# Performance work log

Measured on AMD Instinct MI355X. Metric: run time of the kernel, lower is better.

## Reference

```python
import jax, jax.numpy as jnp
import numpy as np

# ---- config (matches init_kwargs) ----
B, N, D = 16, 300, 256
HEADS, HD = 8, D // 8
FF = 1024
HID = FF // 2                      # SwiGLU hidden
SPATIAL = [(80, 80), (40, 40), (20, 20), (10, 10)]
LVL = len(SPATIAL)
NP = 4                              # points per level
TP = LVL * NP                       # total sampling points = 16
L = sum(h * w for h, w in SPATIAL)  # 8400
EPS = 1e-6


def setup_inputs() -> dict:
    key = jax.random.key(0)
    ks = jax.random.split(key, 24)
    s = 0.02
    return {
        "target": jax.random.normal(ks[0], (B, N, D), jnp.float32),
        "reference_points": jax.random.uniform(ks[1], (B, N, 1, 4), jnp.float32, 0.05, 0.95),
        "memory": jax.random.normal(ks[2], (B, L, D), jnp.float32),
        # self-attention
        "qkv_w": jax.random.normal(ks[3], (3 * D, D), jnp.float32) * s,
        "qkv_b": jnp.zeros((3 * D,), jnp.float32),
        "out_w": jax.random.normal(ks[4], (D, D), jnp.float32) * s,
        "out_b": jnp.zeros((D,), jnp.float32),
        "norm1_w": jnp.ones((D,), jnp.float32),
        # deformable cross-attention
        "off_w": jax.random.normal(ks[5], (HEADS * TP * 2, D), jnp.float32) * s,
        "off_b": jax.random.normal(ks[6], (HEADS * TP * 2,), jnp.float32) * 0.1,
        "aw_w": jax.random.normal(ks[7], (HEADS * TP, D), jnp.float32) * s,
        "aw_b": jnp.zeros((HEADS * TP,), jnp.float32),
        "cout_w": jax.random.normal(ks[8], (D, D), jnp.float32) * s,
        "cout_b": jnp.zeros((D,), jnp.float32),
        "norm2_w": jnp.ones((D,), jnp.float32),
        # SwiGLU FFN
        "w13": jax.random.normal(ks[9], (2 * HID, D), jnp.float32) * s,
        "w13_b": jnp.zeros((2 * HID,), jnp.float32),
        "w2": jax.random.normal(ks[10], (D, HID), jnp.float32) * s,
        "w2_b": jnp.zeros((D,), jnp.float32),
        "norm3_w": jnp.ones((D,), jnp.float32),
    }


def rmsnorm(x, w):
    return x * jax.lax.rsqrt(jnp.mean(x * x, axis=-1, keepdims=True) + EPS) * w


def bilinear_sample(vflat, loc, H, W):
    """vflat: (BH, hd, H*W); loc: (BH, Q, 2) in [0,1]. grid_sample align_corners=False, zero pad."""
    x = loc[..., 0] * W - 0.5
    y = loc[..., 1] * H - 0.5
    x0 = jnp.floor(x); y0 = jnp.floor(y)
    dx = x - x0; dy = y - y0
    x0i = x0.astype(jnp.int32); y0i = y0.astype(jnp.int32)

    def gather(xi, yi, w):
        valid = (xi >= 0) & (xi < W) & (yi >= 0) & (yi < H)
        idx = jnp.clip(yi, 0, H - 1) * W + jnp.clip(xi, 0, W - 1)
        g = jnp.take_along_axis(vflat, idx[:, None, :], axis=2)  # (BH, hd, Q)
        return g * (w * valid)[:, None, :]

    return (gather(x0i, y0i, (1 - dx) * (1 - dy))
            + gather(x0i + 1, y0i, dx * (1 - dy))
            + gather(x0i, y0i + 1, (1 - dx) * dy)
            + gather(x0i + 1, y0i + 1, dx * dy))


def reference(target, reference_points, memory, qkv_w, qkv_b, out_w, out_b, norm1_w,
              off_w, off_b, aw_w, aw_b, cout_w, cout_b, norm2_w,
              w13, w13_b, w2, w2_b, norm3_w):
    # ---------- self-attention (query_pos_embed=None, attn_mask=None) ----------
    qkv = target @ qkv_w.T + qkv_b                    # (B,N,3D)
    qkv = qkv.reshape(B, N, 3, HEADS, HD).transpose(2, 0, 3, 1, 4)
    q, k, v = qkv[0], qkv[1], qkv[2]                  # (B,H,N,hd)
    attn = jax.nn.softmax(jnp.einsum("bhqd,bhkd->bhqk", q, k) / np.sqrt(HD), axis=-1)
    sa = jnp.einsum("bhqk,bhkd->bhqd", attn, v).transpose(0, 2, 1, 3).reshape(B, N, D)
    x = rmsnorm(target + (sa @ out_w.T + out_b), norm1_w)

    # ---------- deformable cross-attention ----------
    # value_op: memory -> per-head value (B,H,hd,L)
    val = memory.reshape(B, L, HEADS, HD).transpose(0, 2, 3, 1).reshape(B * HEADS, HD, L)

    offsets = (x @ off_w.T + off_b).reshape(B, N, HEADS, TP, 2)
    aw = jax.nn.softmax((x @ aw_w.T + aw_b).reshape(B, N, HEADS, TP), axis=-1)

    ref_xy = reference_points[:, :, :, None, :2]      # (B,N,1,1,2)
    ref_wh = reference_points[:, :, :, None, 2:]
    pts_scale = 1.0 / NP
    loc = ref_xy + offsets * pts_scale * ref_wh * 0.5  # (B,N,H,TP,2)
    loc = loc.transpose(0, 2, 1, 3, 4).reshape(B * HEADS, N, TP, 2)

    sampled = []
    start = 0
    for li, (H, W) in enumerate(SPATIAL):
        v_l = jax.lax.dynamic_slice_in_dim(val, start, H * W, axis=2)
        loc_l = loc[:, :, li * NP:(li + 1) * NP, :].reshape(B * HEADS, N * NP, 2)
        s = bilinear_sample(v_l, loc_l, H, W).reshape(B * HEADS, HD, N, NP)
        sampled.append(s)
        start += H * W
    sampled = jnp.concatenate(sampled, axis=-1)        # (BH, hd, N, TP)

    w = aw.transpose(0, 2, 1, 3).reshape(B * HEADS, 1, N, TP)
    ca = (sampled * w).sum(-1)                         # (BH, hd, N)
    ca = ca.reshape(B, HEADS, HD, N).transpose(0, 3, 1, 2).reshape(B, N, D)
    ca = ca @ cout_w.T + cout_b

    x = rmsnorm(x + ca, norm2_w)

    # ---------- SwiGLU FFN ----------
    h = x @ w13.T + w13_b
    h1, h2 = h[..., :HID], h[..., HID:]
    ffn = (jax.nn.silu(h1) * h2) @ w2.T + w2_b
    x = jnp.clip(x + ffn, -65504.0, 65504.0)
    return rmsnorm(x, norm3_w)
```

## Files before the change

### kernel.cpp

```cpp
#include <hip/hip_runtime.h>
#include <cstdint>
#include <cstddef>


typedef __attribute__((ext_vector_type(8))) short bf16x8;
typedef __attribute__((ext_vector_type(4))) float f32x4;

__device__ __forceinline__ unsigned short f2bf(float f) {
  unsigned int u = __float_as_uint(f);
  u = (u + 0x7fffu + ((u >> 16) & 1u)) >> 16;
  return (unsigned short)u;
}
__device__ __forceinline__ float bf2f(unsigned short b) {
  return __uint_as_float(((unsigned int)b) << 16);
}
__device__ __forceinline__ unsigned int pack2bf(float lo, float hi) {
  return ((unsigned int)f2bf(hi) << 16) | (unsigned int)f2bf(lo);
}

__device__ __forceinline__ void gemm_dev(
    const float* __restrict__ A, const float* __restrict__ W,
    const float* __restrict__ bias, float* __restrict__ C,
    int N, int K, int row0, int col0,
    unsigned short* As, unsigned short* Ws)
{
  const int t = threadIdx.x, wave = t >> 6, lane = t & 63;
  const int lr = lane & 15, g = lane >> 4;
  const int sr = t >> 4, sc = (t & 15) * 4;

  float4 ra[4], rw[8];
  const float* Ab = A + (size_t)(row0 + sr) * K + sc;
  const float* Wb = W + (size_t)(col0 + sr) * K + sc;

#pragma unroll
  for (int i = 0; i < 4; ++i) ra[i] = *(const float4*)(Ab + (size_t)16 * i * K);
#pragma unroll
  for (int j = 0; j < 8; ++j) rw[j] = *(const float4*)(Wb + (size_t)16 * j * K);

  f32x4 acc[4][2] = {};

  for (int k0 = 0; k0 < K; k0 += 64) {
    __syncthreads();
#pragma unroll
    for (int i = 0; i < 4; ++i) {
      uint2 p;
      p.x = pack2bf(ra[i].x, ra[i].y);
      p.y = pack2bf(ra[i].z, ra[i].w);
      *(uint2*)&As[(sr + 16 * i) * 72 + sc] = p;
    }
#pragma unroll
    for (int j = 0; j < 8; ++j) {
      uint2 p;
      p.x = pack2bf(rw[j].x, rw[j].y);
      p.y = pack2bf(rw[j].z, rw[j].w);
      *(uint2*)&Ws[(sr + 16 * j) * 72 + sc] = p;
    }
    __syncthreads();

    if (k0 + 64 < K) {
#pragma unroll
      for (int i = 0; i < 4; ++i)
        ra[i] = *(const float4*)(Ab + (size_t)16 * i * K + k0 + 64);
#pragma unroll
      for (int j = 0; j < 8; ++j)
        rw[j] = *(const float4*)(Wb + (size_t)16 * j * K + k0 + 64);
    }

#pragma unroll
    for (int ks = 0; ks < 2; ++ks) {
      bf16x8 aA[4], bB[2];
#pragma unroll
      for (int i = 0; i < 4; ++i)
        aA[i] = *(const bf16x8*)&As[(i * 16 + lr) * 72 + ks * 32 + g * 8];
#pragma unroll
      for (int j = 0; j < 2; ++j)
        bB[j] = *(const bf16x8*)&Ws[(wave * 32 + j * 16 + lr) * 72 + ks * 32 + g * 8];
#pragma unroll
      for (int i = 0; i < 4; ++i)
#pragma unroll
        for (int j = 0; j < 2; ++j)
          acc[i][j] = __builtin_amdgcn_mfma_f32_16x16x32_bf16(aA[i], bB[j], acc[i][j], 0, 0, 0);
    }
  }

  const float b0 = bias[col0 + wave * 32 + lr];
  const float b1 = bias[col0 + wave * 32 + 16 + lr];
#pragma unroll
  for (int i = 0; i < 4; ++i) {
#pragma unroll
    for (int r = 0; r < 4; ++r) {
      const int row = row0 + i * 16 + g * 4 + r;
      float* dst = &C[(size_t)row * N + col0 + wave * 32 + lr];
      dst[0]  = acc[i][0][r] + b0;
      dst[16] = acc[i][1][r] + b1;
    }
  }
}

__global__ __launch_bounds__(256) void gemm_mfma(
    const float* __restrict__ A, const float* __restrict__ W,
    const float* __restrict__ bias, float* __restrict__ C, int N, int K)
{
  __shared__ __align__(16) unsigned short As[64 * 72];
  __shared__ __align__(16) unsigned short Ws[128 * 72];
  gemm_dev(A, W, bias, C, N, K, blockIdx.y * 64, blockIdx.x * 128, As, Ws);
}

__global__ __launch_bounds__(256) void gemm_offaw(
    const float* __restrict__ X,
    const float* __restrict__ off_w, const float* __restrict__ off_b, float* __restrict__ OF,
    const float* __restrict__ aw_w, const float* __restrict__ aw_b, float* __restrict__ AW,
    int K)
{
  __shared__ __align__(16) unsigned short As[64 * 72];
  __shared__ __align__(16) unsigned short Ws[128 * 72];
  if (blockIdx.x < 2)
    gemm_dev(X, off_w, off_b, OF, 256, K, blockIdx.y * 64, blockIdx.x * 128, As, Ws);
  else
    gemm_dev(X, aw_w, aw_b, AW, 128, K, blockIdx.y * 64, 0, As, Ws);
}

__global__ __launch_bounds__(256) void attn_mfma(
    const float* __restrict__ qkv, float* __restrict__ sa)
{
  __shared__ __align__(16) unsigned short Ksh[304 * 40];
  __shared__ __align__(16) unsigned short Vt[32 * 328];
  __shared__ __align__(16) unsigned short Qsh[64 * 40];
  __shared__ __align__(16) unsigned short Pw[4][16 * 40];

  const int bh = blockIdx.y, b = bh >> 3, h = bh & 7;
  const int chunk = blockIdx.x;
  const int q0 = chunk * 64;
  const int t = threadIdx.x, wave = t >> 6, lane = t & 63;
  const int lr = lane & 15, g = lane >> 4;
  const size_t base = (size_t)b * 300 * 768 + (size_t)h * 32;
  const float scale = 0.17677669529663687f;

  for (int i = t; i < 304 * 16; i += 256) {
    int j = i >> 4, cp = (i & 15) * 2;
    float2 v = make_float2(0.f, 0.f);
    if (j < 300) v = *(const float2*)&qkv[base + (size_t)j * 768 + 256 + cp];
    *(unsigned int*)&Ksh[j * 40 + cp] = pack2bf(v.x, v.y);
  }
  for (int i = t; i < 320 * 16; i += 256) {
    int j = i >> 4, cp = (i & 15) * 2;
    float2 v = make_float2(0.f, 0.f);
    if (j < 300) v = *(const float2*)&qkv[base + (size_t)j * 768 + 512 + cp];
    Vt[(size_t)cp * 328 + j] = f2bf(v.x);
    Vt[(size_t)(cp + 1) * 328 + j] = f2bf(v.y);
  }
  for (int i = t; i < 64 * 16; i += 256) {
    int qr = i >> 4, cp = (i & 15) * 2;
    int q = q0 + qr;
    float2 v = make_float2(0.f, 0.f);
    if (q < 300) v = *(const float2*)&qkv[base + (size_t)q * 768 + cp];
    *(unsigned int*)&Qsh[qr * 40 + cp] = pack2bf(v.x * scale, v.y * scale);
  }
  __syncthreads();

  const int gt = chunk * 4 + wave;
  if (gt < 19) {
    unsigned short* P = &Pw[wave][0];

    bf16x8 aQ = *(const bf16x8*)&Qsh[(wave * 16 + lr) * 40 + g * 8];

    f32x4 s[19];
    const f32x4 zero = {0.f, 0.f, 0.f, 0.f};
#pragma unroll
    for (int kt = 0; kt < 19; ++kt) {
      bf16x8 bK = *(const bf16x8*)&Ksh[(kt * 16 + lr) * 40 + g * 8];
      s[kt] = __builtin_amdgcn_mfma_f32_16x16x32_bf16(aQ, bK, zero, 0, 0, 0);
    }
    if (lr >= 12) {
      s[18][0] = -1e30f; s[18][1] = -1e30f; s[18][2] = -1e30f; s[18][3] = -1e30f;
    }

    float inv[4];
#pragma unroll
    for (int r = 0; r < 4; ++r) {
      float m = -1e30f;
#pragma unroll
      for (int kt = 0; kt < 19; ++kt) m = fmaxf(m, s[kt][r]);
#pragma unroll
      for (int o = 8; o >= 1; o >>= 1) m = fmaxf(m, __shfl_xor(m, o));
      float sum = 0.f;
#pragma unroll
      for (int kt = 0; kt < 19; ++kt) {
        float e = __expf(s[kt][r] - m);
        s[kt][r] = e;
        sum += e;
      }
#pragma unroll
      for (int o = 8; o >= 1; o >>= 1) sum += __shfl_xor(sum, o);
      inv[r] = 1.f / sum;
    }

    f32x4 o0 = {0.f, 0.f, 0.f, 0.f}, o1 = {0.f, 0.f, 0.f, 0.f};
#pragma unroll
    for (int ks = 0; ks < 10; ++ks) {
#pragma unroll
      for (int tp = 0; tp < 2; ++tp) {
        const int kt = ks * 2 + tp;
#pragma unroll
        for (int r = 0; r < 4; ++r) {
          unsigned short pv = (kt < 19) ? f2bf(s[kt][r]) : (unsigned short)0;
          P[(g * 4 + r) * 40 + tp * 16 + lr] = pv;
        }
      }
      asm volatile("s_waitcnt lgkmcnt(0)" ::: "memory");
      __builtin_amdgcn_sched_barrier(0);
      bf16x8 aP = *(const bf16x8*)&P[lr * 40 + g * 8];
      bf16x8 bV0 = *(const bf16x8*)&Vt[(size_t)lr * 328 + ks * 32 + g * 8];
      bf16x8 bV1 = *(const bf16x8*)&Vt[(size_t)(16 + lr) * 328 + ks * 32 + g * 8];
      o0 = __builtin_amdgcn_mfma_f32_16x16x32_bf16(aP, bV0, o0, 0, 0, 0);
      o1 = __builtin_amdgcn_mfma_f32_16x16x32_bf16(aP, bV1, o1, 0, 0, 0);
    }

#pragma unroll
    for (int r = 0; r < 4; ++r) {
      int q = gt * 16 + g * 4 + r;
      if (q < 300) {
        float iv = inv[r];
        float* dst = &sa[((size_t)b * 300 + q) * 256 + h * 32];
        dst[lr] = o0[r] * iv;
        dst[16 + lr] = o1[r] * iv;
      }
    }
  }
}

__global__ __launch_bounds__(256) void add_rmsnorm(
    const float* __restrict__ a, const float* __restrict__ bsrc,
    const float* __restrict__ w, float* __restrict__ out, int clip)
{
  __shared__ float red[4];
  const int row = blockIdx.x, t = threadIdx.x;
  const size_t idx = (size_t)row * 256 + t;
  float v = a[idx] + bsrc[idx];
  if (clip) v = fminf(fmaxf(v, -65504.f), 65504.f);
  float s = v * v;
#pragma unroll
  for (int o = 32; o; o >>= 1) s += __shfl_xor(s, o);
  if ((t & 63) == 0) red[t >> 6] = s;
  __syncthreads();
  float tot = red[0] + red[1] + red[2] + red[3];
  out[idx] = v * rsqrtf(tot * (1.0f / 256.0f) + 1e-6f) * w[t];
}

__global__ __launch_bounds__(256) void swiglu_k(
    const float* __restrict__ h, float* __restrict__ hid)
{
  size_t i = (size_t)blockIdx.x * 256 + threadIdx.x;
  int row = (int)(i >> 9), c = (int)(i & 511);
  float a = h[(size_t)row * 1024 + c];
  float g = h[(size_t)row * 1024 + 512 + c];
  hid[i] = a / (1.f + __expf(-a)) * g;
}

__global__ __launch_bounds__(256) void deform_k(
    const float* __restrict__ memory, const float* __restrict__ refp,
    const float* __restrict__ OFF, const float* __restrict__ AW,
    float* __restrict__ ca)
{
  __shared__ float locx[8][16], locy[8][16], wgt[8][16];
  const int bn = blockIdx.x, b = bn / 300, t = threadIdx.x;

  if (t < 128) {
    int h = t >> 4, p = t & 15;
    float cx = refp[(size_t)bn * 4 + 0], cy = refp[(size_t)bn * 4 + 1];
    float rw = refp[(size_t)bn * 4 + 2], rh = refp[(size_t)bn * 4 + 3];
    float ox = OFF[(size_t)bn * 256 + h * 32 + p * 2 + 0];
    float oy = OFF[(size_t)bn * 256 + h * 32 + p * 2 + 1];
    locx[h][p] = cx + ox * 0.125f * rw;
    locy[h][p] = cy + oy * 0.125f * rh;
    float av = AW[(size_t)bn * 128 + t];
    float mx = av;
#pragma unroll
    for (int o = 8; o; o >>= 1) mx = fmaxf(mx, __shfl_xor(mx, o));
    float e = __expf(av - mx);
    float ssum = e;
#pragma unroll
    for (int o = 8; o; o >>= 1) ssum += __shfl_xor(ssum, o);
    wgt[h][p] = e / ssum;
  }
  __syncthreads();

  const int h = t >> 5, hd = t & 31;
  const float* mb = memory + (size_t)b * 8500 * 256 + h * 32 + hd;
  float acc = 0.f;
#pragma unroll
  for (int p = 0; p < 16; ++p) {
    const int HWs[4] = {80, 40, 20, 10};
    const int Sts[4] = {0, 6400, 8000, 8400};
    const int li = p >> 2;
    const int Hh = HWs[li], Ww = HWs[li], st = Sts[li];
    float x = locx[h][p] * (float)Ww - 0.5f;
    float y = locy[h][p] * (float)Hh - 0.5f;
    float x0f = floorf(x), y0f = floorf(y);
    float dx = x - x0f, dy = y - y0f;
    int x0 = (int)x0f, y0 = (int)y0f;
    float awp = wgt[h][p];
#pragma unroll
    for (int cc = 0; cc < 4; ++cc) {
      int xi = x0 + (cc & 1), yi = y0 + (cc >> 1);
      float wc = ((cc & 1) ? dx : 1.f - dx) * ((cc >> 1) ? dy : 1.f - dy);
      bool valid = (xi >= 0) && (xi < Ww) && (yi >= 0) && (yi < Hh);
      int xc = xi < 0 ? 0 : (xi >= Ww ? Ww - 1 : xi);
      int yc = yi < 0 ? 0 : (yi >= Hh ? Hh - 1 : yi);
      float gv = mb[(size_t)(st + yc * Ww + xc) * 256];
      acc += gv * (valid ? wc * awp : 0.f);
    }
  }
  ca[(size_t)bn * 256 + t] = acc;
}

extern "C" void kernel_launch(void* const* d_in, const int* in_sizes, int n_in,
                              void* d_out, int out_size, void* d_ws, size_t ws_size,
                              hipStream_t stream)
{
  (void)in_sizes; (void)n_in; (void)out_size; (void)ws_size;
  const float* target  = (const float*)d_in[0];
  const float* refp    = (const float*)d_in[1];
  const float* memory  = (const float*)d_in[2];
  const float* qkv_w   = (const float*)d_in[3];
  const float* qkv_b   = (const float*)d_in[4];
  const float* out_w   = (const float*)d_in[5];
  const float* out_b   = (const float*)d_in[6];
  const float* norm1_w = (const float*)d_in[7];
  const float* off_w   = (const float*)d_in[8];
  const float* off_b   = (const float*)d_in[9];
  const float* aw_w    = (const float*)d_in[10];
  const float* aw_b    = (const float*)d_in[11];
  const float* cout_w  = (const float*)d_in[12];
  const float* cout_b  = (const float*)d_in[13];
  const float* norm2_w = (const float*)d_in[14];
  const float* w13     = (const float*)d_in[15];
  const float* w13_b   = (const float*)d_in[16];
  const float* w2      = (const float*)d_in[17];
  const float* w2_b    = (const float*)d_in[18];
  const float* norm3_w = (const float*)d_in[19];
  float* out = (float*)d_out;

  float* ws  = (float*)d_ws;
  float* QKV = ws;
  float* SA  = QKV + 4800 * 768;
  float* T1  = SA  + 4800 * 256;
  float* X   = T1  + 4800 * 256;
  float* OF  = X   + 4800 * 256;
  float* AWb = OF  + 4800 * 256;
  float* CA  = AWb + 4800 * 128;
  float* X2  = CA  + 4800 * 256;
  float* Hb  = X2  + 4800 * 256;
  float* HID = Hb  + 4800 * 1024;

  dim3 blk(256);

  gemm_mfma<<<dim3(6, 75), blk, 0, stream>>>(target, qkv_w, qkv_b, QKV, 768, 256);
  attn_mfma<<<dim3(5, 128), blk, 0, stream>>>(QKV, SA);
  gemm_mfma<<<dim3(2, 75), blk, 0, stream>>>(SA, out_w, out_b, T1, 256, 256);
  add_rmsnorm<<<4800, blk, 0, stream>>>(target, T1, norm1_w, X, 0);
  gemm_offaw<<<dim3(3, 75), blk, 0, stream>>>(X, off_w, off_b, OF, aw_w, aw_b, AWb, 256);
  deform_k<<<4800, blk, 0, stream>>>(memory, refp, OF, AWb, CA);
  gemm_mfma<<<dim3(2, 75), blk, 0, stream>>>(CA, cout_w, cout_b, T1, 256, 256);
  add_rmsnorm<<<4800, blk, 0, stream>>>(X, T1, norm2_w, X2, 0);
  gemm_mfma<<<dim3(8, 75), blk, 0, stream>>>(X2, w13, w13_b, Hb, 1024, 256);
  swiglu_k<<<9600, blk, 0, stream>>>(Hb, HID);
  gemm_mfma<<<dim3(2, 75), blk, 0, stream>>>(HID, w2, w2_b, T1, 256, 512);
  add_rmsnorm<<<4800, blk, 0, stream>>>(X2, T1, norm3_w, out, 1);
}
```

Measured before the change: 152.3 us.

## Split self-attention into a bf16 QKV repack kernel and a per-wave attention kernel

The fused attention kernel, where each block re-converted the full K and V of its head into shared memory, is replaced by two kernels. A repack kernel converts Q (pre-scaled), K and transposed V to bf16 once per batch-head into scratch space borrowed from the FFN hidden buffer. A single-wave attention kernel per 16-query tile then reads its MFMA operands straight from global memory instead of LDS. This removes the redundant per-block conversion and the LDS staging barrier, at the cost of an extra launch, a global round trip for the bf16 copies, and uncoalesced operand loads that rely on cache hits.

```diff
diff --git a/kernel.cpp b/kernel.cpp
--- a/kernel.cpp
+++ b/kernel.cpp
@@ -120,111 +120,109 @@
     gemm_dev(X, aw_w, aw_b, AW, 128, K, blockIdx.y * 64, 0, As, Ws);
 }
 
-__global__ __launch_bounds__(256) void attn_mfma(
-    const float* __restrict__ qkv, float* __restrict__ sa)
-{
-  __shared__ __align__(16) unsigned short Ksh[304 * 40];
-  __shared__ __align__(16) unsigned short Vt[32 * 328];
-  __shared__ __align__(16) unsigned short Qsh[64 * 40];
-  __shared__ __align__(16) unsigned short Pw[4][16 * 40];
-
-  const int bh = blockIdx.y, b = bh >> 3, h = bh & 7;
-  const int chunk = blockIdx.x;
-  const int q0 = chunk * 64;
-  const int t = threadIdx.x, wave = t >> 6, lane = t & 63;
-  const int lr = lane & 15, g = lane >> 4;
+__global__ __launch_bounds__(256) void repack_qkv(
+    const float* __restrict__ qkv,
+    unsigned short* __restrict__ Qb, unsigned short* __restrict__ Kb,
+    unsigned short* __restrict__ VTb)
+{
+  const int bh = blockIdx.x, b = bh >> 3, h = bh & 7;
+  const int half = blockIdx.y;
+  const int t = threadIdx.x;
   const size_t base = (size_t)b * 300 * 768 + (size_t)h * 32;
   const float scale = 0.17677669529663687f;
 
-  for (int i = t; i < 304 * 16; i += 256) {
-    int j = i >> 4, cp = (i & 15) * 2;
-    float2 v = make_float2(0.f, 0.f);
-    if (j < 300) v = *(const float2*)&qkv[base + (size_t)j * 768 + 256 + cp];
-    *(unsigned int*)&Ksh[j * 40 + cp] = pack2bf(v.x, v.y);
-  }
-  for (int i = t; i < 320 * 16; i += 256) {
-    int j = i >> 4, cp = (i & 15) * 2;
-    float2 v = make_float2(0.f, 0.f);
-    if (j < 300) v = *(const float2*)&qkv[base + (size_t)j * 768 + 512 + cp];
-    Vt[(size_t)cp * 328 + j] = f2bf(v.x);
-    Vt[(size_t)(cp + 1) * 328 + j] = f2bf(v.y);
-  }
-  for (int i = t; i < 64 * 16; i += 256) {
-    int qr = i >> 4, cp = (i & 15) * 2;
-    int q = q0 + qr;
-    float2 v = make_float2(0.f, 0.f);
-    if (q < 300) v = *(const float2*)&qkv[base + (size_t)q * 768 + cp];
-    *(unsigned int*)&Qsh[qr * 40 + cp] = pack2bf(v.x * scale, v.y * scale);
-  }
-  __syncthreads();
-
-  const int gt = chunk * 4 + wave;
-  if (gt < 19) {
-    unsigned short* P = &Pw[wave][0];
-
-    bf16x8 aQ = *(const bf16x8*)&Qsh[(wave * 16 + lr) * 40 + g * 8];
-
-    f32x4 s[19];
-    const f32x4 zero = {0.f, 0.f, 0.f, 0.f};
+  for (int i = t; i < 152 * 16; i += 256) {
+    const int n = half * 152 + (i >> 4), cp = (i & 15) * 2;
+    float2 q = make_float2(0.f, 0.f), k = make_float2(0.f, 0.f);
+    if (n < 300) {
+      q = *(const float2*)&qkv[base + (size_t)n * 768 + cp];
+      k = *(const float2*)&qkv[base + (size_t)n * 768 + 256 + cp];
+    }
+    *(unsigned int*)&Qb[((size_t)bh * 304 + n) * 32 + cp] = pack2bf(q.x * scale, q.y * scale);
+    *(unsigned int*)&Kb[((size_t)bh * 304 + n) * 32 + cp] = pack2bf(k.x, k.y);
+  }
+  for (int c = half * 16; c < half * 16 + 16; ++c) {
+    for (int n = t; n < 320; n += 256) {
+      float v = (n < 300) ? qkv[base + (size_t)n * 768 + 512 + c] : 0.f;
+      VTb[((size_t)bh * 32 + c) * 320 + n] = f2bf(v);
+    }
+  }
+}
+
+__global__ __launch_bounds__(64) void attn_core(
+    const unsigned short* __restrict__ Qb, const unsigned short* __restrict__ Kb,
+    const unsigned short* __restrict__ VTb, float* __restrict__ sa)
+{
+  __shared__ __align__(16) unsigned short P[16 * 40];
+  const int gt = blockIdx.x;
+  const int bh = blockIdx.y, b = bh >> 3, h = bh & 7;
+  const int lane = threadIdx.x, lr = lane & 15, g = lane >> 4;
+
+  const unsigned short* Kbase = Kb + (size_t)bh * 304 * 32;
+  const unsigned short* Vbase = VTb + (size_t)bh * 32 * 320;
+
+  bf16x8 aQ = *(const bf16x8*)&Qb[((size_t)bh * 304 + gt * 16 + lr) * 32 + g * 8];
+
+  f32x4 s[19];
+  const f32x4 zero = {0.f, 0.f, 0.f, 0.f};
+#pragma unroll
+  for (int kt = 0; kt < 19; ++kt) {
+    bf16x8 bK = *(const bf16x8*)&Kbase[(kt * 16 + lr) * 32 + g * 8];
+    s[kt] = __builtin_amdgcn_mfma_f32_16x16x32_bf16(aQ, bK, zero, 0, 0, 0);
+  }
+  if (lr >= 12) {
+    s[18][0] = -1e30f; s[18][1] = -1e30f; s[18][2] = -1e30f; s[18][3] = -1e30f;
+  }
+
+  float inv[4];
+#pragma unroll
+  for (int r = 0; r < 4; ++r) {
+    float m = -1e30f;
+#pragma unroll
+    for (int kt = 0; kt < 19; ++kt) m = fmaxf(m, s[kt][r]);
+#pragma unroll
+    for (int o = 8; o >= 1; o >>= 1) m = fmaxf(m, __shfl_xor(m, o));
+    float sum = 0.f;
 #pragma unroll
     for (int kt = 0; kt < 19; ++kt) {
-      bf16x8 bK = *(const bf16x8*)&Ksh[(kt * 16 + lr) * 40 + g * 8];
-      s[kt] = __builtin_amdgcn_mfma_f32_16x16x32_bf16(aQ, bK, zero, 0, 0, 0);
-    }
-    if (lr >= 12) {
-      s[18][0] = -1e30f; s[18][1] = -1e30f; s[18][2] = -1e30f; s[18][3] = -1e30f;
-    }
-
-    float inv[4];
-#pragma unroll
-    for (int r = 0; r < 4; ++r) {
-      float m = -1e30f;
-#pragma unroll
-      for (int kt = 0; kt < 19; ++kt) m = fmaxf(m, s[kt][r]);
-#pragma unroll
-      for (int o = 8; o >= 1; o >>= 1) m = fmaxf(m, __shfl_xor(m, o));
-      float sum = 0.f;
-#pragma unroll
-      for (int kt = 0; kt < 19; ++kt) {
-        float e = __expf(s[kt][r] - m);
-        s[kt][r] = e;
-        sum += e;
+      float e = __expf(s[kt][r] - m);
+      s[kt][r] = e;
+      sum += e;
+    }
+#pragma unroll
+    for (int o = 8; o >= 1; o >>= 1) sum += __shfl_xor(sum, o);
+    inv[r] = 1.f / sum;
+  }
+
+  f32x4 o0 = {0.f, 0.f, 0.f, 0.f}, o1 = {0.f, 0.f, 0.f, 0.f};
+#pragma unroll
+  for (int ks = 0; ks < 10; ++ks) {
+#pragma unroll
+    for (int tp = 0; tp < 2; ++tp) {
+      const int kt = ks * 2 + tp;
+#pragma unroll
+      for (int r = 0; r < 4; ++r) {
+        unsigned short pv = (kt < 19) ? f2bf(s[kt][r]) : (unsigned short)0;
+        P[(g * 4 + r) * 40 + tp * 16 + lr] = pv;
       }
-#pragma unroll
-      for (int o = 8; o >= 1; o >>= 1) sum += __shfl_xor(sum, o);
-      inv[r] = 1.f / sum;
-    }
-
-    f32x4 o0 = {0.f, 0.f, 0.f, 0.f}, o1 = {0.f, 0.f, 0.f, 0.f};
-#pragma unroll
-    for (int ks = 0; ks < 10; ++ks) {
-#pragma unroll
-      for (int tp = 0; tp < 2; ++tp) {
-        const int kt = ks * 2 + tp;
-#pragma unroll
-        for (int r = 0; r < 4; ++r) {
-          unsigned short pv = (kt < 19) ? f2bf(s[kt][r]) : (unsigned short)0;
-          P[(g * 4 + r) * 40 + tp * 16 + lr] = pv;
-        }
-      }
-      asm volatile("s_waitcnt lgkmcnt(0)" ::: "memory");
-      __builtin_amdgcn_sched_barrier(0);
-      bf16x8 aP = *(const bf16x8*)&P[lr * 40 + g * 8];
-      bf16x8 bV0 = *(const bf16x8*)&Vt[(size_t)lr * 328 + ks * 32 + g * 8];
-      bf16x8 bV1 = *(const bf16x8*)&Vt[(size_t)(16 + lr) * 328 + ks * 32 + g * 8];
-      o0 = __builtin_amdgcn_mfma_f32_16x16x32_bf16(aP, bV0, o0, 0, 0, 0);
-      o1 = __builtin_amdgcn_mfma_f32_16x16x32_bf16(aP, bV1, o1, 0, 0, 0);
-    }
-
-#pragma unroll
-    for (int r = 0; r < 4; ++r) {
-      int q = gt * 16 + g * 4 + r;
-      if (q < 300) {
-        float iv = inv[r];
-        float* dst = &sa[((size_t)b * 300 + q) * 256 + h * 32];
-        dst[lr] = o0[r] * iv;
-        dst[16 + lr] = o1[r] * iv;
-      }
+    }
+    asm volatile("s_waitcnt lgkmcnt(0)" ::: "memory");
+    __builtin_amdgcn_sched_barrier(0);
+    bf16x8 aP = *(const bf16x8*)&P[lr * 40 + g * 8];
+    bf16x8 bV0 = *(const bf16x8*)&Vbase[(size_t)lr * 320 + ks * 32 + g * 8];
+    bf16x8 bV1 = *(const bf16x8*)&Vbase[(size_t)(16 + lr) * 320 + ks * 32 + g * 8];
+    o0 = __builtin_amdgcn_mfma_f32_16x16x32_bf16(aP, bV0, o0, 0, 0, 0);
+    o1 = __builtin_amdgcn_mfma_f32_16x16x32_bf16(aP, bV1, o1, 0, 0, 0);
+  }
+
+#pragma unroll
+  for (int r = 0; r < 4; ++r) {
+    const int q = gt * 16 + g * 4 + r;
+    if (q < 300) {
+      const float iv = inv[r];
+      float* dst = &sa[((size_t)b * 300 + q) * 256 + h * 32];
+      dst[lr] = o0[r] * iv;
+      dst[16 + lr] = o1[r] * iv;
     }
   }
 }
@@ -353,10 +351,15 @@
   float* Hb  = X2  + 4800 * 256;
   float* HID = Hb  + 4800 * 1024;
 
+  unsigned short* Qb  = (unsigned short*)Hb;
+  unsigned short* Kb  = Qb + 128 * 304 * 32;
+  unsigned short* VTb = Kb + 128 * 304 * 32;
+
   dim3 blk(256);
 
   gemm_mfma<<<dim3(6, 75), blk, 0, stream>>>(target, qkv_w, qkv_b, QKV, 768, 256);
-  attn_mfma<<<dim3(5, 128), blk, 0, stream>>>(QKV, SA);
+  repack_qkv<<<dim3(128, 2), blk, 0, stream>>>(QKV, Qb, Kb, VTb);
+  attn_core<<<dim3(19, 128), dim3(64), 0, stream>>>(Qb, Kb, VTb, SA);
   gemm_mfma<<<dim3(2, 75), blk, 0, stream>>>(SA, out_w, out_b, T1, 256, 256);
   add_rmsnorm<<<4800, blk, 0, stream>>>(target, T1, norm1_w, X, 0);
   gemm_offaw<<<dim3(3, 75), blk, 0, stream>>>(X, off_w, off_b, OF, aw_w, aw_b, AWb, 256);
```

Measured after the change: 144.6 us. -5.1%, faster.
